# Kernel tuning notes

Hardware: AMD Instinct MI355X
Metric: run time of the kernel (lower is better)

Reference implementation:

```python
import jax, jax.numpy as jnp
import numpy as np

G, N, DEG = 64, 2048, 8          # graphs, nodes/graph, avg degree
NTOT = G * N                      # 131072 nodes
E = NTOT * DEG                    # 1048576 edges
K = int(np.ceil(0.2 * N))         # 410 nodes kept per graph (SAGPooling ratio=0.2)
NK = G * K                        # 26240 pooled nodes
H, C = 3, 20                      # GAT heads, per-head channels
NEG_BIG = jnp.float32(-1e30)


def gcn(x, src, dst, W, b, n):
    """PyG GCNConv: x' = D^-1/2 (A+I) D^-1/2 x W + b (edge weight 1)."""
    h = x @ W
    deg = jax.ops.segment_sum(jnp.ones(src.shape[0], x.dtype), dst, num_segments=n) + 1.0
    dinv = jax.lax.rsqrt(deg)
    coef = dinv[src] * dinv[dst]                    # [E]
    agg = jax.ops.segment_sum(h[src] * coef[:, None], dst, num_segments=n)
    agg = agg + h * (dinv * dinv)[:, None]          # self loops
    return agg + b


def setup_inputs() -> dict:
    key = jax.random.key(0)
    ks = jax.random.split(key, 16)
    # edges constrained within each graph: per-graph local indices + offsets
    off = jnp.repeat(jnp.arange(G, dtype=jnp.int32) * N, N * DEG)   # [E]
    src = jax.random.randint(ks[0], (E,), 0, N, dtype=jnp.int32) + off
    dst = jax.random.randint(ks[1], (E,), 0, N, dtype=jnp.int32) + off
    batch = jnp.repeat(jnp.arange(G, dtype=jnp.int32), N)           # [NTOT]
    x = jax.random.normal(ks[2], (NTOT, 5), jnp.float32)
    s = 0.1
    return {
        "x": x, "src": src, "dst": dst, "batch": batch,
        "W1": jax.random.normal(ks[3], (5, 10)) * s,   "b1": jnp.zeros((10,)),
        "Ws": jax.random.normal(ks[4], (10, 1)) * s,   "bs": jnp.zeros((1,)),
        "Wg": jax.random.normal(ks[5], (10, H * C)) * s,
        "a_src": jax.random.normal(ks[6], (H, C)) * s,
        "a_dst": jax.random.normal(ks[7], (H, C)) * s,
        "bg": jnp.zeros((H * C,)),
        "Wf1": jax.random.normal(ks[8], (60, 30)) * s, "bf1": jnp.zeros((30,)),
        "Wf2": jax.random.normal(ks[9], (30, 3)) * s,  "bf2": jnp.zeros((3,)),
    }


def reference(x, src, dst, batch, W1, b1, Ws, bs, Wg, a_src, a_dst, bg, Wf1, bf1, Wf2, bf2):
    n = x.shape[0]
    # GCNConv(5,10)
    x1 = gcn(x, src, dst, W1, b1, n)                              # [NTOT,10]
    # SAGPooling: GCN scorer, top-k per graph, gate by tanh(score)
    score = gcn(x1, src, dst, Ws, bs, n)[:, 0]                    # [NTOT]
    _, topi = jax.lax.top_k(score.reshape(G, N), K)               # [G,K]
    perm = (topi + (jnp.arange(G) * N)[:, None]).reshape(-1)      # [NK] global ids
    xp = x1[perm] * jnp.tanh(score[perm])[:, None]                # [NK,10]
    # remap edges; drop (mask) edges touching removed nodes (filter_adj)
    new_idx = jnp.full((n,), -1, jnp.int32).at[perm].set(jnp.arange(NK, dtype=jnp.int32))
    s2, d2 = new_idx[src], new_idx[dst]
    emask = (s2 >= 0) & (d2 >= 0)
    s2 = jnp.where(emask, s2, 0)
    d2 = jnp.where(emask, d2, 0)
    # GATConv(10, 20, heads=3) with self loops
    h = (xp @ Wg).reshape(NK, H, C)
    al_s = jnp.sum(h * a_src, -1)                                 # [NK,H]
    al_d = jnp.sum(h * a_dst, -1)
    loop = jnp.arange(NK, dtype=jnp.int32)
    sa = jnp.concatenate([s2, loop])
    da = jnp.concatenate([d2, loop])
    ma = jnp.concatenate([emask, jnp.ones((NK,), bool)])
    logits = jax.nn.leaky_relu(al_s[sa] + al_d[da], 0.2)          # [E+NK,H]
    logits = jnp.where(ma[:, None], logits, NEG_BIG)
    mx = jax.ops.segment_max(logits, da, num_segments=NK)         # finite: self loops
    w = jnp.exp(logits - mx[da]) * ma[:, None]
    denom = jax.ops.segment_sum(w, da, num_segments=NK)
    alpha = w / denom[da]                                         # edge softmax
    out = jax.ops.segment_sum(h[sa] * alpha[..., None], da, num_segments=NK)  # [NK,H,C]
    xg = out.reshape(NK, H * C) + bg                              # concat heads -> 60
    # scatter_add readout over graphs
    g = jax.ops.segment_sum(xg, batch[perm], num_segments=G)      # [G,60]
    # MLP + LogSoftmax
    z = jax.nn.relu(g @ Wf1 + bf1) @ Wf2 + bf2                    # [G,3]
    return jax.nn.log_softmax(z, axis=1)
```

## Files before the change

kernel.cpp:

```cpp
#include <hip/hip_runtime.h>
#include <math.h>

#define G    64
#define NPG  2048
#define NTOT (G * NPG)
#define EPG  (NPG * 8)
#define NE   (NTOT * 8)
#define KSEL 410
#define NH   3
#define NC   20
#define HC   60
#define FCAP 24
#define KPAD 512
#define RP   12

#define OFF_H1P   0
#define OFF_CSR   98304
#define OFF_HIST  131072
#define OFF_RS    139264
#define OFF_SK    147456
#define OFF_NEWL  155648
#define OFF_PERML 159744
#define OFF_WSUM  160568
#define OFF_FLAGS 160632
#define ARENA_SZ  160648
#define OFF_XP    0
#define OFF_FADJ  16400
#define OFF_FCNT  36080
#define OFF_HF    37728
#define OFF_ALS   139264
#define OFF_ALD   144184
#define OFF_WRED  149104
#define OFF_GOUT  151024
#define OFF_HID   151264

__device__ inline float leaky(float x) { return x >= 0.f ? x : 0.2f * x; }

__device__ inline int wave_incl_scan(int v) {
    int lane = threadIdx.x & 63;
#pragma unroll
    for (int d = 1; d < 64; d <<= 1) {
        int t = __shfl_up(v, d, 64);
        if (lane >= d) v += t;
    }
    return v;
}

__global__ __launch_bounds__(1024) void k_all(
    const float* __restrict__ x, const int* __restrict__ src, const int* __restrict__ dst,
    const float* __restrict__ W1, const float* __restrict__ b1,
    const float* __restrict__ Ws, const float* __restrict__ bs,
    const float* __restrict__ Wg, const float* __restrict__ a_srcw,
    const float* __restrict__ a_dstw, const float* __restrict__ bg,
    const float* __restrict__ Wf1, const float* __restrict__ bf1,
    const float* __restrict__ Wf2, const float* __restrict__ bf2,
    float* __restrict__ x1g, float* __restrict__ out)
{
    __shared__ __align__(16) char arena[ARENA_SZ];
    float*          h1p   = (float*)(arena + OFF_H1P);
    unsigned short* csrL  = (unsigned short*)(arena + OFF_CSR);
    int*            hist  = (int*)(arena + OFF_HIST);
    int*            rsL   = (int*)(arena + OFF_RS);
    unsigned*       skL   = (unsigned*)(arena + OFF_SK);
    unsigned short* newLs = (unsigned short*)(arena + OFF_NEWL);
    unsigned short* permL = (unsigned short*)(arena + OFF_PERML);
    int*            wsumL = (int*)(arena + OFF_WSUM);
    int*            flags = (int*)(arena + OFF_FLAGS);
    float*          xpL   = (float*)(arena + OFF_XP);
    unsigned short* fadjL = (unsigned short*)(arena + OFF_FADJ);
    int*            fcntL = (int*)(arena + OFF_FCNT);
    float*          hfL   = (float*)(arena + OFF_HF);
    float*          alsL  = (float*)(arena + OFF_ALS);
    float*          aldL  = (float*)(arena + OFF_ALD);
    float*          wred  = (float*)(arena + OFF_WRED);
    float*          goutL = (float*)(arena + OFF_GOUT);
    float*          hidL  = (float*)(arena + OFF_HID);
#define bselS  flags[0]
#define bneedS flags[1]
#define curS   flags[2]
#define totS   flags[3]

    int g = blockIdx.x, tid = threadIdx.x, wid = tid >> 6;
    int nbase = g * NPG, ebase = g * EPG;

    for (int i = tid; i < NPG; i += 1024) hist[i] = 0;
    for (int i = tid; i < NPG; i += 1024) {
        float xi[5];
#pragma unroll
        for (int k = 0; k < 5; k++) xi[k] = x[(size_t)(nbase + i) * 5 + k];
        float v[10];
#pragma unroll
        for (int j = 0; j < 10; j++) {
            float s = 0.f;
#pragma unroll
            for (int k = 0; k < 5; k++) s += xi[k] * W1[k * 10 + j];
            v[j] = s;
        }
        float4* row = (float4*)(h1p + i * RP);
        row[0] = make_float4(v[0], v[1], v[2], v[3]);
        row[1] = make_float4(v[4], v[5], v[6], v[7]);
        row[2] = make_float4(v[8], v[9], 0.f, 0.f);
    }
    __syncthreads();
    for (int e = tid; e < EPG; e += 1024)
        atomicAdd(&hist[dst[ebase + e] - nbase], 1);
    __syncthreads();
    {
        int b2 = tid * 2;
        int v0 = hist[b2], v1 = hist[b2 + 1];
        int s = v0 + v1;
        int incl = wave_incl_scan(s);
        if ((tid & 63) == 63) wsumL[wid] = incl;
        __syncthreads();
        if (tid == 0) {
            int a = 0;
#pragma unroll
            for (int w = 0; w < 16; w++) { int t = wsumL[w]; wsumL[w] = a; a += t; }
        }
        __syncthreads();
        int base = wsumL[wid] + incl - s;
        rsL[b2] = base;
        rsL[b2 + 1] = base + v0;
        h1p[b2 * RP + 10] = rsqrtf((float)v0 + 1.0f);
        h1p[(b2 + 1) * RP + 10] = rsqrtf((float)v1 + 1.0f);
        hist[b2] = 0; hist[b2 + 1] = 0;
    }
    __syncthreads();
    for (int e = tid; e < EPG; e += 1024) {
        int ee = ebase + e;
        int sl = src[ee] - nbase;
        int dl = dst[ee] - nbase;
        int pos = rsL[dl] + atomicAdd(&hist[dl], 1);
        csrL[pos] = (unsigned short)sl;
    }
    __syncthreads();

    for (int i = tid; i < NPG; i += 1024) {
        const float4* rowi = (const float4*)(h1p + i * RP);
        float4 s0 = rowi[0], s1 = rowi[1], s2 = rowi[2];
        float di = s2.z;
        float a0 = 0.f, a1 = 0.f, a2 = 0.f, a3 = 0.f, a4 = 0.f;
        float a5 = 0.f, a6 = 0.f, a7 = 0.f, a8 = 0.f, a9 = 0.f;
        int p0 = rsL[i], p1 = (i == NPG - 1) ? EPG : rsL[i + 1];
        for (int e = p0; e < p1; e++) {
            int s = csrL[e];
            const float4* rw = (const float4*)(h1p + s * RP);
            float4 r0 = rw[0], r1 = rw[1], r2 = rw[2];
            float dv = r2.z;
            a0 += r0.x * dv; a1 += r0.y * dv; a2 += r0.z * dv; a3 += r0.w * dv;
            a4 += r1.x * dv; a5 += r1.y * dv; a6 += r1.z * dv; a7 += r1.w * dv;
            a8 += r2.x * dv; a9 += r2.y * dv;
        }
        float d2 = di * di;
        float v[10];
        v[0] = a0 * di + s0.x * d2 + b1[0];
        v[1] = a1 * di + s0.y * d2 + b1[1];
        v[2] = a2 * di + s0.z * d2 + b1[2];
        v[3] = a3 * di + s0.w * d2 + b1[3];
        v[4] = a4 * di + s1.x * d2 + b1[4];
        v[5] = a5 * di + s1.y * d2 + b1[5];
        v[6] = a6 * di + s1.z * d2 + b1[6];
        v[7] = a7 * di + s1.w * d2 + b1[7];
        v[8] = a8 * di + s2.x * d2 + b1[8];
        v[9] = a9 * di + s2.y * d2 + b1[9];
        float dot = 0.f;
#pragma unroll
        for (int j = 0; j < 10; j++) dot += v[j] * Ws[j];
        float4* xr = (float4*)(x1g + (size_t)(nbase + i) * RP);
        xr[0] = make_float4(v[0], v[1], v[2], v[3]);
        xr[1] = make_float4(v[4], v[5], v[6], v[7]);
        xr[2] = make_float4(v[8], v[9], 0.f, 0.f);
        h1p[i * RP + 11] = dot;
    }
    __syncthreads();

    float bsv = bs[0];
    for (int i = tid; i < NPG; i += 1024) {
        float2 own = *(const float2*)(h1p + i * RP + 10);
        int p0 = rsL[i], p1 = (i == NPG - 1) ? EPG : rsL[i + 1];
        float a = 0.f;
        for (int e = p0; e < p1; e++) {
            float2 dh = *(const float2*)(h1p + csrL[e] * RP + 10);
            a += dh.x * dh.y;
        }
        float sc = own.x * a + own.y * own.x * own.x + bsv;
        unsigned u = __float_as_uint(sc);
        skL[i] = (u & 0x80000000u) ? ~u : (u | 0x80000000u);
        newLs[i] = 0xFFFFu;
        hist[i] = 0;
    }
    if (tid == 0) curS = 0;
    int need = KSEL;
    unsigned prefix = 0;
    __syncthreads();

    for (int lv = 0; lv < 3; lv++) {
        for (int i = tid; i < NPG; i += 1024) {
            unsigned k = skL[i];
            bool match; unsigned bb;
            if (lv == 0)      { match = true;                  bb = k >> 21; }
            else if (lv == 1) { match = ((k >> 21) == prefix); bb = (k >> 10) & 0x7FFu; }
            else              { match = ((k >> 10) == prefix); bb = k & 0x3FFu; }
            if (match) atomicAdd(&hist[bb], 1);
        }
        __syncthreads();
        int b2 = tid * 2;
        int v0 = hist[b2], v1 = hist[b2 + 1];
        hist[b2] = 0; hist[b2 + 1] = 0;
        int s = v0 + v1;
        int incl = wave_incl_scan(s);
        if ((tid & 63) == 63) wsumL[wid] = incl;
        __syncthreads();
        if (tid == 0) {
            int a = 0;
#pragma unroll
            for (int w = 0; w < 16; w++) { int t = wsumL[w]; wsumL[w] = a; a += t; }
            totS = a;
        }
        __syncthreads();
        int base = wsumL[wid] + incl - s;
        int tot = totS;
        { int Sb = tot - base;        int Sb1 = Sb - v0; if (Sb >= need && Sb1 < need) { bselS = b2;     bneedS = need - Sb1; } }
        { int Sb = tot - (base + v0); int Sb1 = Sb - v1; if (Sb >= need && Sb1 < need) { bselS = b2 + 1; bneedS = need - Sb1; } }
        __syncthreads();
        if (lv == 0)      prefix = (unsigned)bselS;
        else if (lv == 1) prefix = (prefix << 11) | (unsigned)bselS;
        else              prefix = (prefix << 10) | (unsigned)bselS;
        need = bneedS;
        __syncthreads();
    }
    unsigned T = prefix;
    int greaterCnt = KSEL - need;

    for (int i = tid; i < NPG; i += 1024) {
        if (skL[i] > T) {
            int p = atomicAdd(&curS, 1);
            permL[p] = (unsigned short)i;
            newLs[i] = (unsigned short)p;
        }
    }
    {
        int b2 = tid * 2;
        int lc = 0, loc2[2];
#pragma unroll
        for (int k = 0; k < 2; k++)
            if (skL[b2 + k] == T) loc2[lc++] = b2 + k;
        __syncthreads();
        int incl = wave_incl_scan(lc);
        if ((tid & 63) == 63) wsumL[wid] = incl;
        __syncthreads();
        if (tid == 0) {
            int a = 0;
#pragma unroll
            for (int w = 0; w < 16; w++) { int t = wsumL[w]; wsumL[w] = a; a += t; }
        }
        __syncthreads();
        int rank0 = wsumL[wid] + incl - lc;
        for (int j = 0; j < lc; j++) {
            int rank = rank0 + j;
            if (rank < need) {
                int p = greaterCnt + rank;
                permL[p] = (unsigned short)loc2[j];
                newLs[loc2[j]] = (unsigned short)p;
            }
        }
    }
    __syncthreads();

    for (int p = tid; p < KSEL; p += 1024) {
        int iL = permL[p];
        unsigned k = skL[iL];
        unsigned u = (k & 0x80000000u) ? (k & 0x7FFFFFFFu) : ~k;
        float tt = tanhf(__uint_as_float(u));
        const float4* xr = (const float4*)(x1g + (size_t)(nbase + iL) * RP);
        float4 q0 = xr[0], q1 = xr[1], q2 = xr[2];
        float* xp = xpL + p * 10;
        xp[0] = q0.x * tt; xp[1] = q0.y * tt; xp[2] = q0.z * tt; xp[3] = q0.w * tt;
        xp[4] = q1.x * tt; xp[5] = q1.y * tt; xp[6] = q1.z * tt; xp[7] = q1.w * tt;
        xp[8] = q2.x * tt; xp[9] = q2.y * tt;
        int p0 = rsL[iL], p1 = (iL == NPG - 1) ? EPG : rsL[iL + 1];
        int c = 0;
        for (int e = p0; e < p1; e++) {
            unsigned short s2 = newLs[csrL[e]];
            if (s2 != 0xFFFFu && c < FCAP) fadjL[p * FCAP + c++] = s2;
        }
        fcntL[p] = c;
    }
    __syncthreads();

    for (int t = tid; t < KSEL * NH; t += 1024) {
        int p = t / NH, hh = t - p * NH;
        float xi[10];
#pragma unroll
        for (int k = 0; k < 10; k++) xi[k] = xpL[p * 10 + k];
        float v[NC];
        float as_ = 0.f, ad_ = 0.f;
#pragma unroll
        for (int c = 0; c < NC; c++) {
            int j = hh * NC + c;
            float vv = 0.f;
#pragma unroll
            for (int k = 0; k < 10; k++) vv += xi[k] * Wg[k * HC + j];
            v[c] = vv;
            as_ += vv * a_srcw[j];
            ad_ += vv * a_dstw[j];
        }
        float4* hr = (float4*)(hfL + p * HC + hh * NC);
#pragma unroll
        for (int q = 0; q < 5; q++)
            hr[q] = make_float4(v[4 * q], v[4 * q + 1], v[4 * q + 2], v[4 * q + 3]);
        alsL[p * NH + hh] = as_;
        aldL[p * NH + hh] = ad_;
    }
    __syncthreads();

    {
        float res[NC];
#pragma unroll
        for (int rnd = 0; rnd < 2; rnd++) {
            int task = rnd == 0 ? tid : 1024 + tid;
            bool on = rnd == 0 || tid < KPAD;
            int hh = task >> 9, p = task & (KPAD - 1);
            if (on) {
                if (p < KSEL) {
                    float aldp = aldL[p * NH + hh];
                    float lself = leaky(alsL[p * NH + hh] + aldp);
                    float m = lself;
                    int c = fcntL[p];
                    const unsigned short* f = fadjL + p * FCAP;
                    for (int e = 0; e < c; e++)
                        m = fmaxf(m, leaky(alsL[f[e] * NH + hh] + aldp));
                    float wself = expf(lself - m), wsum = wself;
                    const float4* hp = (const float4*)(hfL + p * HC + hh * NC);
                    float4 r0 = hp[0], r1 = hp[1], r2 = hp[2], r3 = hp[3], r4 = hp[4];
                    r0.x *= wself; r0.y *= wself; r0.z *= wself; r0.w *= wself;
                    r1.x *= wself; r1.y *= wself; r1.z *= wself; r1.w *= wself;
                    r2.x *= wself; r2.y *= wself; r2.z *= wself; r2.w *= wself;
                    r3.x *= wself; r3.y *= wself; r3.z *= wself; r3.w *= wself;
                    r4.x *= wself; r4.y *= wself; r4.z *= wself; r4.w *= wself;
                    for (int e = 0; e < c; e++) {
                        int s2 = f[e];
                        float w = expf(leaky(alsL[s2 * NH + hh] + aldp) - m);
                        wsum += w;
                        const float4* hq = (const float4*)(hfL + s2 * HC + hh * NC);
                        float4 t0 = hq[0], t1 = hq[1], t2 = hq[2], t3 = hq[3], t4 = hq[4];
                        r0.x += w * t0.x; r0.y += w * t0.y; r0.z += w * t0.z; r0.w += w * t0.w;
                        r1.x += w * t1.x; r1.y += w * t1.y; r1.z += w * t1.z; r1.w += w * t1.w;
                        r2.x += w * t2.x; r2.y += w * t2.y; r2.z += w * t2.z; r2.w += w * t2.w;
                        r3.x += w * t3.x; r3.y += w * t3.y; r3.z += w * t3.z; r3.w += w * t3.w;
                        r4.x += w * t4.x; r4.y += w * t4.y; r4.z += w * t4.z; r4.w += w * t4.w;
                    }
                    float inv = 1.f / wsum;
                    res[0] = r0.x * inv; res[1] = r0.y * inv; res[2] = r0.z * inv; res[3] = r0.w * inv;
                    res[4] = r1.x * inv; res[5] = r1.y * inv; res[6] = r1.z * inv; res[7] = r1.w * inv;
                    res[8] = r2.x * inv; res[9] = r2.y * inv; res[10] = r2.z * inv; res[11] = r2.w * inv;
                    res[12] = r3.x * inv; res[13] = r3.y * inv; res[14] = r3.z * inv; res[15] = r3.w * inv;
                    res[16] = r4.x * inv; res[17] = r4.y * inv; res[18] = r4.z * inv; res[19] = r4.w * inv;
                } else {
#pragma unroll
                    for (int cc = 0; cc < NC; cc++) res[cc] = 0.f;
                }
#pragma unroll
                for (int cc = 0; cc < NC; cc++) {
                    float v = res[cc];
#pragma unroll
                    for (int d = 1; d < 64; d <<= 1) v += __shfl_xor(v, d, 64);
                    res[cc] = v;
                }
                if ((tid & 63) == 0) {
                    int slot = rnd == 0 ? hh * 8 + (wid & 7) : 16 + wid;
#pragma unroll
                    for (int cc = 0; cc < NC; cc++) wred[slot * NC + cc] = res[cc];
                }
            }
        }
    }
    __syncthreads();
    if (tid < HC) {
        int hh = tid / NC, c = tid - hh * NC;
        float a = 0.f;
#pragma unroll
        for (int w = 0; w < 8; w++) a += wred[(hh * 8 + w) * NC + c];
        goutL[tid] = a + (float)KSEL * bg[tid];
    }
    __syncthreads();

    if (tid < 30) {
        float s = bf1[tid];
#pragma unroll
        for (int k = 0; k < HC; k++) s += goutL[k] * Wf1[k * 30 + tid];
        hidL[tid] = s > 0.f ? s : 0.f;
    }
    __syncthreads();
    if (tid == 0) {
        float z[3];
#pragma unroll
        for (int j = 0; j < 3; j++) {
            float s = bf2[j];
            for (int k = 0; k < 30; k++) s += hidL[k] * Wf2[k * 3 + j];
            z[j] = s;
        }
        float m = fmaxf(z[0], fmaxf(z[1], z[2]));
        float lse = logf(expf(z[0] - m) + expf(z[1] - m) + expf(z[2] - m)) + m;
#pragma unroll
        for (int j = 0; j < 3; j++) out[g * 3 + j] = z[j] - lse;
    }
}

extern "C" void kernel_launch(void* const* d_in, const int* in_sizes, int n_in,
                              void* d_out, int out_size, void* d_ws, size_t ws_size,
                              hipStream_t stream) {
    const float* x     = (const float*)d_in[0];
    const int*   src   = (const int*)d_in[1];
    const int*   dst   = (const int*)d_in[2];
    const float* W1    = (const float*)d_in[4];
    const float* b1    = (const float*)d_in[5];
    const float* Ws    = (const float*)d_in[6];
    const float* bs    = (const float*)d_in[7];
    const float* Wg    = (const float*)d_in[8];
    const float* a_src = (const float*)d_in[9];
    const float* a_dst = (const float*)d_in[10];
    const float* bg    = (const float*)d_in[11];
    const float* Wf1   = (const float*)d_in[12];
    const float* bf1   = (const float*)d_in[13];
    const float* Wf2   = (const float*)d_in[14];
    const float* bf2   = (const float*)d_in[15];
    float* out = (float*)d_out;

    float* x1g = (float*)d_ws;

    k_all<<<G, 1024, 0, stream>>>(x, src, dst, W1, b1, Ws, bs, Wg, a_src, a_dst,
                                  bg, Wf1, bf1, Wf2, bf2, x1g, out);
}
```

Before: 143.5 us.

## Compute GCN layer-1 output only for kept nodes, fold scorer weights algebraically

The SAG scorer now uses linearity: x1·Ws is obtained by aggregating the precomputed h·Ws scalar, so the full 10-wide layer-1 aggregation over all 2048 nodes is dropped. It is now computed only for the 410 selected nodes, held in registers, and the global x1 scratch buffer is removed. Edges are read once into packed registers and reused for both the histogram and the CSR fill. The filtered adjacency list is gone; the GAT pass filters the CSR on the fly through newLs. Row starts are stored as 16-bit values. The risks are an extra block-wide sync for the scorer, more divergent CSR walks inside the GAT loop, and higher register pressure.

```diff
diff --git a/kernel.cpp b/kernel.cpp
--- a/kernel.cpp
+++ b/kernel.cpp
@@ -10,29 +10,26 @@
 #define NH   3
 #define NC   20
 #define HC   60
-#define FCAP 24
 #define KPAD 512
 #define RP   12
 
 #define OFF_H1P   0
-#define OFF_CSR   98304
-#define OFF_HIST  131072
+#define OFF_HF    0
+#define OFF_HIST  98304
+#define OFF_ALD   98400
+#define OFF_CSR   106496
 #define OFF_RS    139264
-#define OFF_SK    147456
-#define OFF_NEWL  155648
-#define OFF_PERML 159744
-#define OFF_WSUM  160568
-#define OFF_FLAGS 160632
-#define ARENA_SZ  160648
-#define OFF_XP    0
-#define OFF_FADJ  16400
-#define OFF_FCNT  36080
-#define OFF_HF    37728
-#define OFF_ALS   139264
-#define OFF_ALD   144184
-#define OFF_WRED  149104
-#define OFF_GOUT  151024
-#define OFF_HID   151264
+#define OFF_HSL   143368
+#define OFF_NEWL  143368
+#define OFF_SK    151560
+#define OFF_ALS   151560
+#define OFF_PERML 159752
+#define OFF_WRED  160576
+#define OFF_HID   160576
+#define OFF_GOUT  162496
+#define OFF_WSUM  162736
+#define OFF_FLAGS 162800
+#define ARENA_SZ  162816
 
 __device__ inline float leaky(float x) { return x >= 0.f ? x : 0.2f * x; }
 
@@ -54,27 +51,25 @@
     const float* __restrict__ a_dstw, const float* __restrict__ bg,
     const float* __restrict__ Wf1, const float* __restrict__ bf1,
     const float* __restrict__ Wf2, const float* __restrict__ bf2,
-    float* __restrict__ x1g, float* __restrict__ out)
+    float* __restrict__ out)
 {
     __shared__ __align__(16) char arena[ARENA_SZ];
     float*          h1p   = (float*)(arena + OFF_H1P);
+    float*          hfL   = (float*)(arena + OFF_HF);
+    int*            hist  = (int*)(arena + OFF_HIST);
+    float*          aldL  = (float*)(arena + OFF_ALD);
     unsigned short* csrL  = (unsigned short*)(arena + OFF_CSR);
-    int*            hist  = (int*)(arena + OFF_HIST);
-    int*            rsL   = (int*)(arena + OFF_RS);
+    unsigned short* rsL   = (unsigned short*)(arena + OFF_RS);
+    float*          hsLf  = (float*)(arena + OFF_HSL);
+    unsigned short* newLs = (unsigned short*)(arena + OFF_NEWL);
     unsigned*       skL   = (unsigned*)(arena + OFF_SK);
-    unsigned short* newLs = (unsigned short*)(arena + OFF_NEWL);
+    float*          alsL  = (float*)(arena + OFF_ALS);
     unsigned short* permL = (unsigned short*)(arena + OFF_PERML);
+    float*          wred  = (float*)(arena + OFF_WRED);
+    float*          hidL  = (float*)(arena + OFF_HID);
+    float*          goutL = (float*)(arena + OFF_GOUT);
     int*            wsumL = (int*)(arena + OFF_WSUM);
     int*            flags = (int*)(arena + OFF_FLAGS);
-    float*          xpL   = (float*)(arena + OFF_XP);
-    unsigned short* fadjL = (unsigned short*)(arena + OFF_FADJ);
-    int*            fcntL = (int*)(arena + OFF_FCNT);
-    float*          hfL   = (float*)(arena + OFF_HF);
-    float*          alsL  = (float*)(arena + OFF_ALS);
-    float*          aldL  = (float*)(arena + OFF_ALD);
-    float*          wred  = (float*)(arena + OFF_WRED);
-    float*          goutL = (float*)(arena + OFF_GOUT);
-    float*          hidL  = (float*)(arena + OFF_HID);
 #define bselS  flags[0]
 #define bneedS flags[1]
 #define curS   flags[2]
@@ -89,21 +84,29 @@
 #pragma unroll
         for (int k = 0; k < 5; k++) xi[k] = x[(size_t)(nbase + i) * 5 + k];
         float v[10];
+        float hw = 0.f;
 #pragma unroll
         for (int j = 0; j < 10; j++) {
             float s = 0.f;
 #pragma unroll
             for (int k = 0; k < 5; k++) s += xi[k] * W1[k * 10 + j];
             v[j] = s;
+            hw += s * Ws[j];
         }
         float4* row = (float4*)(h1p + i * RP);
         row[0] = make_float4(v[0], v[1], v[2], v[3]);
         row[1] = make_float4(v[4], v[5], v[6], v[7]);
-        row[2] = make_float4(v[8], v[9], 0.f, 0.f);
-    }
-    __syncthreads();
-    for (int e = tid; e < EPG; e += 1024)
-        atomicAdd(&hist[dst[ebase + e] - nbase], 1);
+        row[2] = make_float4(v[8], v[9], 0.f, hw);
+    }
+    unsigned epack[16];
+#pragma unroll
+    for (int k = 0; k < 16; k++) {
+        int ee = ebase + tid + k * 1024;
+        int sl = src[ee] - nbase;
+        int dl = dst[ee] - nbase;
+        epack[k] = ((unsigned)sl << 16) | (unsigned)dl;
+        atomicAdd(&hist[dl], 1);
+    }
     __syncthreads();
     {
         int b2 = tid * 2;
@@ -116,77 +119,52 @@
             int a = 0;
 #pragma unroll
             for (int w = 0; w < 16; w++) { int t = wsumL[w]; wsumL[w] = a; a += t; }
+            rsL[NPG] = (unsigned short)EPG;
         }
         __syncthreads();
         int base = wsumL[wid] + incl - s;
-        rsL[b2] = base;
-        rsL[b2 + 1] = base + v0;
+        rsL[b2] = (unsigned short)base;
+        rsL[b2 + 1] = (unsigned short)(base + v0);
         h1p[b2 * RP + 10] = rsqrtf((float)v0 + 1.0f);
         h1p[(b2 + 1) * RP + 10] = rsqrtf((float)v1 + 1.0f);
         hist[b2] = 0; hist[b2 + 1] = 0;
     }
     __syncthreads();
-    for (int e = tid; e < EPG; e += 1024) {
-        int ee = ebase + e;
-        int sl = src[ee] - nbase;
-        int dl = dst[ee] - nbase;
-        int pos = rsL[dl] + atomicAdd(&hist[dl], 1);
+#pragma unroll
+    for (int k = 0; k < 16; k++) {
+        int dl = epack[k] & 0xFFFFu, sl = epack[k] >> 16;
+        int pos = (int)rsL[dl] + atomicAdd(&hist[dl], 1);
         csrL[pos] = (unsigned short)sl;
     }
     __syncthreads();
 
-    for (int i = tid; i < NPG; i += 1024) {
-        const float4* rowi = (const float4*)(h1p + i * RP);
-        float4 s0 = rowi[0], s1 = rowi[1], s2 = rowi[2];
-        float di = s2.z;
-        float a0 = 0.f, a1 = 0.f, a2 = 0.f, a3 = 0.f, a4 = 0.f;
-        float a5 = 0.f, a6 = 0.f, a7 = 0.f, a8 = 0.f, a9 = 0.f;
-        int p0 = rsL[i], p1 = (i == NPG - 1) ? EPG : rsL[i + 1];
-        for (int e = p0; e < p1; e++) {
-            int s = csrL[e];
-            const float4* rw = (const float4*)(h1p + s * RP);
-            float4 r0 = rw[0], r1 = rw[1], r2 = rw[2];
-            float dv = r2.z;
-            a0 += r0.x * dv; a1 += r0.y * dv; a2 += r0.z * dv; a3 += r0.w * dv;
-            a4 += r1.x * dv; a5 += r1.y * dv; a6 += r1.z * dv; a7 += r1.w * dv;
-            a8 += r2.x * dv; a9 += r2.y * dv;
-        }
-        float d2 = di * di;
-        float v[10];
-        v[0] = a0 * di + s0.x * d2 + b1[0];
-        v[1] = a1 * di + s0.y * d2 + b1[1];
-        v[2] = a2 * di + s0.z * d2 + b1[2];
-        v[3] = a3 * di + s0.w * d2 + b1[3];
-        v[4] = a4 * di + s1.x * d2 + b1[4];
-        v[5] = a5 * di + s1.y * d2 + b1[5];
-        v[6] = a6 * di + s1.z * d2 + b1[6];
-        v[7] = a7 * di + s1.w * d2 + b1[7];
-        v[8] = a8 * di + s2.x * d2 + b1[8];
-        v[9] = a9 * di + s2.y * d2 + b1[9];
-        float dot = 0.f;
-#pragma unroll
-        for (int j = 0; j < 10; j++) dot += v[j] * Ws[j];
-        float4* xr = (float4*)(x1g + (size_t)(nbase + i) * RP);
-        xr[0] = make_float4(v[0], v[1], v[2], v[3]);
-        xr[1] = make_float4(v[4], v[5], v[6], v[7]);
-        xr[2] = make_float4(v[8], v[9], 0.f, 0.f);
-        h1p[i * RP + 11] = dot;
-    }
-    __syncthreads();
-
-    float bsv = bs[0];
+    float bw = 0.f;
+#pragma unroll
+    for (int j = 0; j < 10; j++) bw += b1[j] * Ws[j];
     for (int i = tid; i < NPG; i += 1024) {
         float2 own = *(const float2*)(h1p + i * RP + 10);
-        int p0 = rsL[i], p1 = (i == NPG - 1) ? EPG : rsL[i + 1];
+        int p0 = rsL[i], p1 = rsL[i + 1];
         float a = 0.f;
         for (int e = p0; e < p1; e++) {
             float2 dh = *(const float2*)(h1p + csrL[e] * RP + 10);
             a += dh.x * dh.y;
         }
-        float sc = own.x * a + own.y * own.x * own.x + bsv;
+        hsLf[i] = own.x * a + own.y * own.x * own.x + bw;
+    }
+    __syncthreads();
+
+    float bsv = bs[0];
+    for (int i = tid; i < NPG; i += 1024) {
+        float di = h1p[i * RP + 10];
+        int p0 = rsL[i], p1 = rsL[i + 1];
+        float a = 0.f;
+        for (int e = p0; e < p1; e++) {
+            int s = csrL[e];
+            a += h1p[s * RP + 10] * hsLf[s];
+        }
+        float sc = di * a + hsLf[i] * di * di + bsv;
         unsigned u = __float_as_uint(sc);
         skL[i] = (u & 0x80000000u) ? ~u : (u | 0x80000000u);
-        newLs[i] = 0xFFFFu;
         hist[i] = 0;
     }
     if (tid == 0) curS = 0;
@@ -196,6 +174,7 @@
 
     for (int lv = 0; lv < 3; lv++) {
         for (int i = tid; i < NPG; i += 1024) {
+            if (lv == 0) newLs[i] = 0xFFFFu;
             unsigned k = skL[i];
             bool match; unsigned bb;
             if (lv == 0)      { match = true;                  bb = k >> 21; }
@@ -267,50 +246,58 @@
     }
     __syncthreads();
 
-    for (int p = tid; p < KSEL; p += 1024) {
-        int iL = permL[p];
+    float xp[10];
+    bool haveP = tid < KSEL;
+    if (haveP) {
+        int iL = permL[tid];
+        float di = h1p[iL * RP + 10];
+        float a0 = 0.f, a1 = 0.f, a2 = 0.f, a3 = 0.f, a4 = 0.f;
+        float a5 = 0.f, a6 = 0.f, a7 = 0.f, a8 = 0.f, a9 = 0.f;
+        int p0 = rsL[iL], p1 = rsL[iL + 1];
+        for (int e = p0; e < p1; e++) {
+            const float4* rw = (const float4*)(h1p + csrL[e] * RP);
+            float4 r0 = rw[0], r1 = rw[1], r2 = rw[2];
+            float dv = r2.z;
+            a0 += r0.x * dv; a1 += r0.y * dv; a2 += r0.z * dv; a3 += r0.w * dv;
+            a4 += r1.x * dv; a5 += r1.y * dv; a6 += r1.z * dv; a7 += r1.w * dv;
+            a8 += r2.x * dv; a9 += r2.y * dv;
+        }
+        const float4* ro = (const float4*)(h1p + iL * RP);
+        float4 s0 = ro[0], s1 = ro[1], s2 = ro[2];
+        float d2 = di * di;
         unsigned k = skL[iL];
         unsigned u = (k & 0x80000000u) ? (k & 0x7FFFFFFFu) : ~k;
         float tt = tanhf(__uint_as_float(u));
-        const float4* xr = (const float4*)(x1g + (size_t)(nbase + iL) * RP);
-        float4 q0 = xr[0], q1 = xr[1], q2 = xr[2];
-        float* xp = xpL + p * 10;
-        xp[0] = q0.x * tt; xp[1] = q0.y * tt; xp[2] = q0.z * tt; xp[3] = q0.w * tt;
-        xp[4] = q1.x * tt; xp[5] = q1.y * tt; xp[6] = q1.z * tt; xp[7] = q1.w * tt;
-        xp[8] = q2.x * tt; xp[9] = q2.y * tt;
-        int p0 = rsL[iL], p1 = (iL == NPG - 1) ? EPG : rsL[iL + 1];
-        int c = 0;
-        for (int e = p0; e < p1; e++) {
-            unsigned short s2 = newLs[csrL[e]];
-            if (s2 != 0xFFFFu && c < FCAP) fadjL[p * FCAP + c++] = s2;
-        }
-        fcntL[p] = c;
-    }
-    __syncthreads();
-
-    for (int t = tid; t < KSEL * NH; t += 1024) {
-        int p = t / NH, hh = t - p * NH;
-        float xi[10];
-#pragma unroll
-        for (int k = 0; k < 10; k++) xi[k] = xpL[p * 10 + k];
-        float v[NC];
-        float as_ = 0.f, ad_ = 0.f;
-#pragma unroll
-        for (int c = 0; c < NC; c++) {
-            int j = hh * NC + c;
-            float vv = 0.f;
-#pragma unroll
-            for (int k = 0; k < 10; k++) vv += xi[k] * Wg[k * HC + j];
-            v[c] = vv;
-            as_ += vv * a_srcw[j];
-            ad_ += vv * a_dstw[j];
-        }
-        float4* hr = (float4*)(hfL + p * HC + hh * NC);
-#pragma unroll
-        for (int q = 0; q < 5; q++)
-            hr[q] = make_float4(v[4 * q], v[4 * q + 1], v[4 * q + 2], v[4 * q + 3]);
-        alsL[p * NH + hh] = as_;
-        aldL[p * NH + hh] = ad_;
+        xp[0] = (a0 * di + s0.x * d2 + b1[0]) * tt;
+        xp[1] = (a1 * di + s0.y * d2 + b1[1]) * tt;
+        xp[2] = (a2 * di + s0.z * d2 + b1[2]) * tt;
+        xp[3] = (a3 * di + s0.w * d2 + b1[3]) * tt;
+        xp[4] = (a4 * di + s1.x * d2 + b1[4]) * tt;
+        xp[5] = (a5 * di + s1.y * d2 + b1[5]) * tt;
+        xp[6] = (a6 * di + s1.z * d2 + b1[6]) * tt;
+        xp[7] = (a7 * di + s1.w * d2 + b1[7]) * tt;
+        xp[8] = (a8 * di + s2.x * d2 + b1[8]) * tt;
+        xp[9] = (a9 * di + s2.y * d2 + b1[9]) * tt;
+    }
+    __syncthreads();
+
+    if (haveP) {
+        int p = tid;
+        for (int hh = 0; hh < NH; hh++) {
+            float as_ = 0.f, ad_ = 0.f;
+#pragma unroll
+            for (int c = 0; c < NC; c++) {
+                int j = hh * NC + c;
+                float vv = 0.f;
+#pragma unroll
+                for (int k = 0; k < 10; k++) vv += xp[k] * Wg[k * HC + j];
+                hfL[p * HC + j] = vv;
+                as_ += vv * a_srcw[j];
+                ad_ += vv * a_dstw[j];
+            }
+            alsL[p * NH + hh] = as_;
+            aldL[p * NH + hh] = ad_;
+        }
     }
     __syncthreads();
 
@@ -319,17 +306,20 @@
 #pragma unroll
         for (int rnd = 0; rnd < 2; rnd++) {
             int task = rnd == 0 ? tid : 1024 + tid;
-            bool on = rnd == 0 || tid < KPAD;
+            bool on = (rnd == 0) || (tid < KPAD);
             int hh = task >> 9, p = task & (KPAD - 1);
             if (on) {
                 if (p < KSEL) {
+                    int iL = permL[p];
+                    int p0 = rsL[iL], p1 = rsL[iL + 1];
                     float aldp = aldL[p * NH + hh];
                     float lself = leaky(alsL[p * NH + hh] + aldp);
                     float m = lself;
-                    int c = fcntL[p];
-                    const unsigned short* f = fadjL + p * FCAP;
-                    for (int e = 0; e < c; e++)
-                        m = fmaxf(m, leaky(alsL[f[e] * NH + hh] + aldp));
+                    for (int e = p0; e < p1; e++) {
+                        unsigned short s2 = newLs[csrL[e]];
+                        if (s2 != 0xFFFFu)
+                            m = fmaxf(m, leaky(alsL[s2 * NH + hh] + aldp));
+                    }
                     float wself = expf(lself - m), wsum = wself;
                     const float4* hp = (const float4*)(hfL + p * HC + hh * NC);
                     float4 r0 = hp[0], r1 = hp[1], r2 = hp[2], r3 = hp[3], r4 = hp[4];
@@ -338,8 +328,9 @@
                     r2.x *= wself; r2.y *= wself; r2.z *= wself; r2.w *= wself;
                     r3.x *= wself; r3.y *= wself; r3.z *= wself; r3.w *= wself;
                     r4.x *= wself; r4.y *= wself; r4.z *= wself; r4.w *= wself;
-                    for (int e = 0; e < c; e++) {
-                        int s2 = f[e];
+                    for (int e = p0; e < p1; e++) {
+                        unsigned short s2 = newLs[csrL[e]];
+                        if (s2 == 0xFFFFu) continue;
                         float w = expf(leaky(alsL[s2 * NH + hh] + aldp) - m);
                         wsum += w;
                         const float4* hq = (const float4*)(hfL + s2 * HC + hh * NC);
@@ -351,9 +342,9 @@
                         r4.x += w * t4.x; r4.y += w * t4.y; r4.z += w * t4.z; r4.w += w * t4.w;
                     }
                     float inv = 1.f / wsum;
-                    res[0] = r0.x * inv; res[1] = r0.y * inv; res[2] = r0.z * inv; res[3] = r0.w * inv;
-                    res[4] = r1.x * inv; res[5] = r1.y * inv; res[6] = r1.z * inv; res[7] = r1.w * inv;
-                    res[8] = r2.x * inv; res[9] = r2.y * inv; res[10] = r2.z * inv; res[11] = r2.w * inv;
+                    res[0] = r0.x * inv;  res[1] = r0.y * inv;  res[2] = r0.z * inv;  res[3] = r0.w * inv;
+                    res[4] = r1.x * inv;  res[5] = r1.y * inv;  res[6] = r1.z * inv;  res[7] = r1.w * inv;
+                    res[8] = r2.x * inv;  res[9] = r2.y * inv;  res[10] = r2.z * inv; res[11] = r2.w * inv;
                     res[12] = r3.x * inv; res[13] = r3.y * inv; res[14] = r3.z * inv; res[15] = r3.w * inv;
                     res[16] = r4.x * inv; res[17] = r4.y * inv; res[18] = r4.z * inv; res[19] = r4.w * inv;
                 } else {
@@ -427,8 +418,6 @@
     const float* bf2   = (const float*)d_in[15];
     float* out = (float*)d_out;
 
-    float* x1g = (float*)d_ws;
-
     k_all<<<G, 1024, 0, stream>>>(x, src, dst, W1, b1, Ws, bs, Wg, a_src, a_dst,
-                                  bg, Wf1, bf1, Wf2, bf2, x1g, out);
+                                  bg, Wf1, bf1, Wf2, bf2, out);
 }
```

New measurement: 151.8 us. +5.8%, slower.
